# Kernel optimization log

Hardware: AMD Instinct MI355X
Metric: run time of the kernel (lower is better)

Reference implementation:

```python
import jax, jax.numpy as jnp
import numpy as np

B, L, D, H = 2, 2048, 768, 12
HD = D // H  # 64
BASE = 10000


def rope_tables(seq_len, head_dim, base):
    # inverse frequencies over even indices, angles [L, hd/2] -> duplicated to [L, hd]
    inv_freq = 1.0 / (base ** (jnp.arange(0, head_dim, 2, dtype=jnp.float32) / head_dim))
    angles = jnp.arange(seq_len, dtype=jnp.float32)[:, None] * inv_freq[None, :]
    cos = jnp.concatenate([jnp.cos(angles), jnp.cos(angles)], axis=-1)  # [L, hd]
    sin = jnp.concatenate([jnp.sin(angles), jnp.sin(angles)], axis=-1)
    return cos, sin


def rotate_half(x):
    x1, x2 = jnp.split(x, 2, axis=-1)
    return jnp.concatenate([-x2, x1], axis=-1)


def setup_inputs() -> dict:
    key = jax.random.key(0)
    k0, k1, k2 = jax.random.split(key, 3)
    s = 0.02
    return {
        "input_embeddings": jax.random.normal(k0, (B, L, D), dtype=jnp.float32),
        "w_qkv": jax.random.normal(k1, (D, 3 * D), dtype=jnp.float32) * s,
        "b_qkv": jnp.zeros((3 * D,), dtype=jnp.float32),
        "w_out": jax.random.normal(k2, (D, D), dtype=jnp.float32) * s,
        "b_out": jnp.zeros((D,), dtype=jnp.float32),
    }


def reference(input_embeddings, w_qkv, b_qkv, w_out, b_out):
    # QKV projection and head split: b l (h d) -> b h l d
    qkv = input_embeddings @ w_qkv + b_qkv
    q, k, v = jnp.split(qkv, 3, axis=-1)
    to_heads = lambda t: t.reshape(B, L, H, HD).transpose(0, 2, 1, 3)
    q, k, v = map(to_heads, (q, k, v))

    # RoPE (start_pos=0, no kv cache)
    cos, sin = rope_tables(L, HD, BASE)  # [L, HD], broadcasts over b,h
    q = q * cos + rotate_half(q) * sin
    k = k * cos + rotate_half(k) * sin

    # NOTE: source divides by sqrt(d.size(3)) = sqrt(key_seq_len), not sqrt(head_dim)
    scores = jnp.einsum("bhqd,bhkd->bhqk", q, k) / jnp.sqrt(jnp.float32(L))

    causal_mask = jnp.triu(jnp.ones((L, L), dtype=bool), 1)
    neg_inf = -jnp.finfo(scores.dtype).max
    scores = jnp.where(causal_mask, neg_inf, scores)

    probs = jax.nn.softmax(scores, axis=-1)  # dropout disabled (eval)
    attn_out = jnp.einsum("bhqk,bhkd->bhqd", probs, v)
    attn_out = attn_out.transpose(0, 2, 1, 3).reshape(B, L, D)  # b h l d -> b l (h d)
    output = attn_out @ w_out + b_out
    return output, probs
```

## Files before the change

kernel.cpp:

```cpp
#include <hip/hip_runtime.h>
#include <math.h>

#define B_  2
#define L_  2048
#define D_  768
#define H_  12
#define HD_ 64
#define M_  (B_*L_)
#define N3_ (3*D_)
#define OUT_ELEMS ((size_t)B_*L_*D_)

static constexpr float kScale = 0.022097086912079608f;
static constexpr float kLog2_10000_div32 = 0.415241011860920f;

typedef __attribute__((ext_vector_type(8))) short short8;
typedef __attribute__((ext_vector_type(4))) float f32x4;
typedef __attribute__((ext_vector_type(4))) unsigned short us4;

__device__ __forceinline__ unsigned short f2bf(float f) {
  union { float f; unsigned u; } v; v.f = f;
  unsigned r = v.u + 0x7FFFu + ((v.u >> 16) & 1u);
  return (unsigned short)(r >> 16);
}

__device__ __forceinline__ void async_cp16(const void* g, void* l) {
  __builtin_amdgcn_global_load_lds((const __attribute__((address_space(1))) void*)g,
                                   (__attribute__((address_space(3))) void*)l, 16, 0, 0);
}

__global__ __launch_bounds__(256) void bf16conv_kernel(const float* __restrict__ in,
                                                       unsigned short* __restrict__ out)
{
  const int idx = blockIdx.x * 256 + threadIdx.x;
  const float* src = in + (size_t)idx * 8;
  float4 a = *(const float4*)src;
  float4 b = *(const float4*)(src + 4);
  unsigned short t[8];
  t[0] = f2bf(a.x); t[1] = f2bf(a.y); t[2] = f2bf(a.z); t[3] = f2bf(a.w);
  t[4] = f2bf(b.x); t[5] = f2bf(b.y); t[6] = f2bf(b.z); t[7] = f2bf(b.w);
  *(uint4*)(out + (size_t)idx * 8) = *(uint4*)t;
}

__global__ __launch_bounds__(256) void wtrans_kernel(const float* __restrict__ in,
                                                     unsigned short* __restrict__ out,
                                                     int K, int N)
{
  __shared__ __align__(16) unsigned short T[64][72];
  const int n0 = blockIdx.x * 64;
  const int k0 = blockIdx.y * 64;
  const int tid = threadIdx.x;
  const int row = tid >> 2;
  const int col = (tid & 3) * 16;
  {
    const float* src = in + (size_t)(k0 + row) * N + n0 + col;
    unsigned short tmp[16];
#pragma unroll
    for (int j = 0; j < 16; j += 4) {
      float4 v = *(const float4*)(src + j);
      tmp[j] = f2bf(v.x); tmp[j + 1] = f2bf(v.y); tmp[j + 2] = f2bf(v.z); tmp[j + 3] = f2bf(v.w);
    }
    *(uint4*)&T[row][col]     = *(uint4*)tmp;
    *(uint4*)&T[row][col + 8] = *(uint4*)(tmp + 8);
  }
  __syncthreads();
  unsigned short tmp[16];
#pragma unroll
  for (int j = 0; j < 16; ++j) tmp[j] = T[col + j][row];
  unsigned short* dst = out + (size_t)(n0 + row) * K + k0 + col;
  *(uint4*)dst       = *(uint4*)tmp;
  *(uint4*)(dst + 8) = *(uint4*)(tmp + 8);
}

__global__ __launch_bounds__(256) void vtrans_kernel(const unsigned short* __restrict__ vb,
                                                     unsigned short* __restrict__ vt)
{
  __shared__ __align__(16) unsigned short T[64][72];
  const int bh = blockIdx.y;
  const int l0 = blockIdx.x * 64;
  const int tid = threadIdx.x;
  const int row = tid >> 2;
  const int col = (tid & 3) * 16;
  {
    const unsigned short* src = vb + ((size_t)bh * L_ + l0 + row) * HD_ + col;
    *(uint4*)&T[row][col]     = *(const uint4*)src;
    *(uint4*)&T[row][col + 8] = *(const uint4*)(src + 8);
  }
  __syncthreads();
  unsigned short tmp[16];
#pragma unroll
  for (int j = 0; j < 16; ++j) tmp[j] = T[col + j][row];
  unsigned short* dst = vt + ((size_t)bh * HD_ + row) * L_ + l0 + col;
  *(uint4*)dst       = *(uint4*)tmp;
  *(uint4*)(dst + 8) = *(uint4*)(tmp + 8);
}

__global__ __launch_bounds__(256) void gemm_mfma_kernel(
    const unsigned short* __restrict__ A, const unsigned short* __restrict__ Bt,
    const float* __restrict__ bias, float* __restrict__ C,
    int M, int N, int K, int mode,
    unsigned short* __restrict__ qp, unsigned short* __restrict__ kp,
    unsigned short* __restrict__ vp)
{
  __shared__ __align__(16) unsigned short As[2][128 * 32];
  __shared__ __align__(16) unsigned short Bs[2][128 * 32];

  const int tid  = threadIdx.x;
  const int w    = tid >> 6;
  const int lane = tid & 63;
  const int m16  = lane & 15;
  const int quad = lane >> 4;
  const int wr   = w & 1;
  const int wc   = w >> 1;

  const int bm = blockIdx.y * 128;
  const int bn = blockIdx.x * 128;

  const int s0 = w * 128 + lane;
  const int s1 = s0 + 64;
  const int r0 = s0 >> 2, c0 = (s0 & 3) ^ (r0 & 3);
  const int r1 = s1 >> 2, c1 = (s1 & 3) ^ (r1 & 3);
  const unsigned short* gA0 = A + (size_t)(bm + r0) * K + c0 * 8;
  const unsigned short* gA1 = A + (size_t)(bm + r1) * K + c1 * 8;
  const unsigned short* gB0 = Bt + (size_t)(bn + r0) * K + c0 * 8;
  const unsigned short* gB1 = Bt + (size_t)(bn + r1) * K + c1 * 8;
  const int oS0 = (w * 128) * 8;
  const int oS1 = (w * 128 + 64) * 8;

  const int sw = quad ^ (m16 & 3);
  int offA[4], offB[4];
#pragma unroll
  for (int i = 0; i < 4; ++i) {
    const int ra = wr * 64 + i * 16 + m16;
    const int rb = wc * 64 + i * 16 + m16;
    offA[i] = ra * 32 + sw * 8;
    offB[i] = rb * 32 + sw * 8;
  }

  f32x4 acc[4][4];
#pragma unroll
  for (int i = 0; i < 4; ++i)
#pragma unroll
    for (int j = 0; j < 4; ++j) { acc[i][j][0] = 0.f; acc[i][j][1] = 0.f; acc[i][j][2] = 0.f; acc[i][j][3] = 0.f; }

  async_cp16(gA0, &As[0][oS0]);
  async_cp16(gA1, &As[0][oS1]);
  async_cp16(gB0, &Bs[0][oS0]);
  async_cp16(gB1, &Bs[0][oS1]);
  __syncthreads();

  int cur = 0;
  for (int k0 = 0; k0 < K; k0 += 32) {
    const int nk = k0 + 32;
    if (nk < K) {
      unsigned short* an = &As[cur ^ 1][0];
      unsigned short* bn2 = &Bs[cur ^ 1][0];
      async_cp16(gA0 + nk, an + oS0);
      async_cp16(gA1 + nk, an + oS1);
      async_cp16(gB0 + nk, bn2 + oS0);
      async_cp16(gB1 + nk, bn2 + oS1);
    }
    const unsigned short* Ac = &As[cur][0];
    const unsigned short* Bc = &Bs[cur][0];
    short8 af[4], bfr[4];
#pragma unroll
    for (int i = 0; i < 4; ++i) {
      af[i]  = *(const short8*)(Ac + offA[i]);
      bfr[i] = *(const short8*)(Bc + offB[i]);
    }
#pragma unroll
    for (int i = 0; i < 4; ++i)
#pragma unroll
      for (int j = 0; j < 4; ++j)
        acc[i][j] = __builtin_amdgcn_mfma_f32_16x16x32_bf16(af[i], bfr[j], acc[i][j], 0, 0, 0);
    __syncthreads();
    cur ^= 1;
  }

  if (mode == 0) {
#pragma unroll
    for (int j = 0; j < 4; ++j) {
      const int n = bn + wc * 64 + j * 16 + m16;
      const float bj = bias[n];
#pragma unroll
      for (int i = 0; i < 4; ++i) {
        const int mrow = bm + wr * 64 + i * 16 + quad * 4;
#pragma unroll
        for (int r2 = 0; r2 < 4; ++r2)
          C[(size_t)(mrow + r2) * N + n] = acc[i][j][r2] + bj;
      }
    }
  } else {
    const int segbase = bn + wc * 64;
    const int which = segbase / D_;
    const int h = (segbase - which * D_) >> 6;
    unsigned short* dstT = (which == 0) ? qp : (which == 1) ? kp : vp;
    float bj[4];
#pragma unroll
    for (int og = 0; og < 4; ++og) bj[og] = bias[segbase + og * 16 + m16];
    const float invfA = exp2f(-(float)m16 * kLog2_10000_div32);
    const float invfB = exp2f(-(float)(16 + m16) * kLog2_10000_div32);

#pragma unroll
    for (int i = 0; i < 4; ++i) {
      const int mrow = bm + wr * 64 + i * 16 + quad * 4;
#pragma unroll
      for (int r2 = 0; r2 < 4; ++r2) {
        const int m = mrow + r2;
        const int bi = m >> 11;
        const int li = m & (L_ - 1);
        float vals[4];
#pragma unroll
        for (int og = 0; og < 4; ++og) vals[og] = acc[i][og][r2] + bj[og];
        unsigned short* drow = dstT + (((size_t)(bi * H_ + h)) * L_ + li) * HD_;
        if (which == 2) {
#pragma unroll
          for (int og = 0; og < 4; ++og) drow[og * 16 + m16] = f2bf(vals[og]);
        } else {
          const float fl = (float)li;
#pragma unroll
          for (int og = 0; og < 4; ++og) {
            const int d = og * 16 + m16;
            const float theta = fl * ((og & 1) ? invfB : invfA);
            float sv, cv;
            __sincosf(theta, &sv, &cv);
            const float part = vals[og ^ 2];
            const float rot = (og < 2) ? -part : part;
            drow[d] = f2bf(vals[og] * cv + rot * sv);
          }
        }
      }
    }
  }
}

__global__ __launch_bounds__(256) void attn_mfma_kernel(
    const unsigned short* __restrict__ qb, const unsigned short* __restrict__ kb,
    const unsigned short* __restrict__ vt, float* __restrict__ probs,
    unsigned short* __restrict__ attnb)
{
  __shared__ __align__(16) unsigned short Ks[2][64 * 64];
  __shared__ __align__(16) unsigned short Vs[2][64 * 64];
  __shared__ __align__(16) unsigned short Pb[4][16][72];

  const int tid  = threadIdx.x;
  const int w    = tid >> 6;
  const int lane = tid & 63;
  const int m16  = lane & 15;
  const int quad = lane >> 4;

  const int bh = blockIdx.y;
  const int qt = (int)gridDim.x - 1 - (int)blockIdx.x;
  const int q0 = qt * 64;
  const int bb = bh / H_;
  const int hh = bh - bb * H_;
  const int ktiles = qt + 1;
  const int qrow_base = q0 + w * 16;
  const int qrow = qrow_base + m16;

  const unsigned short* kbase = kb + (size_t)bh * L_ * HD_;
  const unsigned short* vbase = vt + (size_t)bh * HD_ * L_;

  const unsigned short* qp = qb + ((size_t)bh * L_ + qrow) * HD_ + quad * 8;
  const short8 qf0 = *(const short8*)(qp);
  const short8 qf1 = *(const short8*)(qp + 32);

  const int s0g = tid, s1g = tid + 256;
  const int r0 = s0g >> 3, c0 = (s0g & 7) ^ (r0 & 7);
  const int r1 = s1g >> 3, c1 = (s1g & 7) ^ (r1 & 7);
  const unsigned short* gK0 = kbase + (size_t)r0 * HD_ + c0 * 8;
  const unsigned short* gK1 = kbase + (size_t)r1 * HD_ + c1 * 8;
  const unsigned short* gV0 = vbase + (size_t)r0 * L_ + c0 * 8;
  const unsigned short* gV1 = vbase + (size_t)r1 * L_ + c1 * 8;
  const int oL0 = (w * 64) * 8;
  const int oL1 = (256 + w * 64) * 8;
  const int swk = m16 & 7;

  float lsum = 0.f;
  {
    async_cp16(gK0, &Ks[0][oL0]);
    async_cp16(gK1, &Ks[0][oL1]);
    __syncthreads();
    int cur = 0;
    for (int kt = 0; kt < ktiles; ++kt) {
      const int k0 = kt * 64;
      if (kt + 1 < ktiles) {
        const size_t adv = (size_t)(kt + 1) * 64 * HD_;
        async_cp16(gK0 + adv, &Ks[cur ^ 1][oL0]);
        async_cp16(gK1 + adv, &Ks[cur ^ 1][oL1]);
      }
      const unsigned short* Kc = &Ks[cur][0];
#pragma unroll
      for (int cg = 0; cg < 4; ++cg) {
        const int r = cg * 16 + m16;
        const short8 b0 = *(const short8*)(Kc + r * 64 + ((quad ^ swk) * 8));
        const short8 b1 = *(const short8*)(Kc + r * 64 + (((quad + 4) ^ swk) * 8));
        f32x4 s = {0.f, 0.f, 0.f, 0.f};
        s = __builtin_amdgcn_mfma_f32_16x16x32_bf16(b0, qf0, s, 0, 0, 0);
        s = __builtin_amdgcn_mfma_f32_16x16x32_bf16(b1, qf1, s, 0, 0, 0);
        const int kb2 = k0 + cg * 16 + quad * 4;
#pragma unroll
        for (int r2 = 0; r2 < 4; ++r2) {
          const float e = __expf(s[r2] * kScale);
          lsum += (kb2 + r2 <= qrow) ? e : 0.f;
        }
      }
      __syncthreads();
      cur ^= 1;
    }
  }
  lsum += __shfl_xor(lsum, 16, 64);
  lsum += __shfl_xor(lsum, 32, 64);
  const float linv = 1.f / lsum;

  f32x4 oacc[4];
#pragma unroll
  for (int og = 0; og < 4; ++og) { oacc[og][0]=0.f; oacc[og][1]=0.f; oacc[og][2]=0.f; oacc[og][3]=0.f; }

  float* const prow = probs + ((size_t)bh * L_ + qrow) * L_;

  {
    async_cp16(gK0, &Ks[0][oL0]);
    async_cp16(gK1, &Ks[0][oL1]);
    async_cp16(gV0, &Vs[0][oL0]);
    async_cp16(gV1, &Vs[0][oL1]);
    __syncthreads();
    int cur = 0;
    for (int kt = 0; kt < ktiles; ++kt) {
      const int k0 = kt * 64;
      if (kt + 1 < ktiles) {
        const size_t advK = (size_t)(kt + 1) * 64 * HD_;
        const int advV = (kt + 1) * 64;
        async_cp16(gK0 + advK, &Ks[cur ^ 1][oL0]);
        async_cp16(gK1 + advK, &Ks[cur ^ 1][oL1]);
        async_cp16(gV0 + advV, &Vs[cur ^ 1][oL0]);
        async_cp16(gV1 + advV, &Vs[cur ^ 1][oL1]);
      }
      const unsigned short* Kc = &Ks[cur][0];
      const unsigned short* Vc = &Vs[cur][0];
#pragma unroll
      for (int cg = 0; cg < 4; ++cg) {
        const int r = cg * 16 + m16;
        const short8 b0 = *(const short8*)(Kc + r * 64 + ((quad ^ swk) * 8));
        const short8 b1 = *(const short8*)(Kc + r * 64 + (((quad + 4) ^ swk) * 8));
        f32x4 s = {0.f, 0.f, 0.f, 0.f};
        s = __builtin_amdgcn_mfma_f32_16x16x32_bf16(b0, qf0, s, 0, 0, 0);
        s = __builtin_amdgcn_mfma_f32_16x16x32_bf16(b1, qf1, s, 0, 0, 0);
        const int cb = cg * 16 + quad * 4;
        const int kb2 = k0 + cb;
        f32x4 pv;
        us4 pb;
#pragma unroll
        for (int r2 = 0; r2 < 4; ++r2) {
          const float p = (kb2 + r2 <= qrow) ? __expf(s[r2] * kScale) * linv : 0.f;
          pv[r2] = p;
          pb[r2] = f2bf(p);
        }
        *(f32x4*)(prow + kb2) = pv;
        *(us4*)(&Pb[w][m16][cb]) = pb;
      }
      const short8 pa0 = *(const short8*)&Pb[w][m16][quad * 8];
      const short8 pa1 = *(const short8*)&Pb[w][m16][32 + quad * 8];
      __builtin_amdgcn_s_setprio(1);
#pragma unroll
      for (int og = 0; og < 4; ++og) {
        const int r = og * 16 + m16;
        const short8 v0 = *(const short8*)(Vc + r * 64 + ((quad ^ swk) * 8));
        const short8 v1 = *(const short8*)(Vc + r * 64 + (((quad + 4) ^ swk) * 8));
        oacc[og] = __builtin_amdgcn_mfma_f32_16x16x32_bf16(v0, pa0, oacc[og], 0, 0, 0);
        oacc[og] = __builtin_amdgcn_mfma_f32_16x16x32_bf16(v1, pa1, oacc[og], 0, 0, 0);
      }
      __builtin_amdgcn_s_setprio(0);
      __syncthreads();
      cur ^= 1;
    }
  }

#pragma unroll
  for (int og = 0; og < 4; ++og) {
    us4 o4;
#pragma unroll
    for (int r2 = 0; r2 < 4; ++r2) o4[r2] = f2bf(oacc[og][r2]);
    *(us4*)(attnb + ((size_t)bb * L_ + qrow) * D_ + hh * HD_ + og * 16 + quad * 4) = o4;
  }

  {
    const f32x4 z4 = {0.f, 0.f, 0.f, 0.f};
    for (int c0z = ktiles * 64; c0z < L_; c0z += 64) {
#pragma unroll
      for (int j = 0; j < 4; ++j)
        *(f32x4*)(prow + c0z + j * 16 + quad * 4) = z4;
    }
  }
}

extern "C" void kernel_launch(void* const* d_in, const int* in_sizes, int n_in,
                              void* d_out, int out_size, void* d_ws, size_t ws_size,
                              hipStream_t stream)
{
  const float* x     = (const float*)d_in[0];
  const float* w_qkv = (const float*)d_in[1];
  const float* b_qkv = (const float*)d_in[2];
  const float* w_out = (const float*)d_in[3];
  const float* b_out = (const float*)d_in[4];

  float* out   = (float*)d_out;
  float* probs = out + OUT_ELEMS;

  const size_t NE = (size_t)B_ * H_ * L_ * HD_;
  unsigned short* qbw   = (unsigned short*)d_ws;
  unsigned short* kbw   = qbw + NE;
  unsigned short* vbw   = kbw + NE;
  unsigned short* vtw   = vbw + NE;
  unsigned short* xbw   = vtw + NE;
  unsigned short* attnb = xbw + NE;
  unsigned short* wqT   = attnb + NE;
  unsigned short* woT   = wqT + (size_t)N3_ * D_;

  bf16conv_kernel<<<(int)(OUT_ELEMS / 8 / 256), 256, 0, stream>>>(x, xbw);
  wtrans_kernel<<<dim3(N3_ / 64, D_ / 64), 256, 0, stream>>>(w_qkv, wqT, D_, N3_);
  wtrans_kernel<<<dim3(D_ / 64, D_ / 64), 256, 0, stream>>>(w_out, woT, D_, D_);

  gemm_mfma_kernel<<<dim3(N3_ / 128, M_ / 128), 256, 0, stream>>>(
      xbw, wqT, b_qkv, nullptr, M_, N3_, D_, 1, qbw, kbw, vbw);

  vtrans_kernel<<<dim3(L_ / 64, B_ * H_), 256, 0, stream>>>(vbw, vtw);

  attn_mfma_kernel<<<dim3(L_ / 64, B_ * H_), 256, 0, stream>>>(qbw, kbw, vtw, probs, attnb);

  gemm_mfma_kernel<<<dim3(D_ / 128, M_ / 128), 256, 0, stream>>>(
      attnb, woT, b_out, out, M_, D_, D_, 0, nullptr, nullptr, nullptr);
}
```

Baseline: 550.5 us.

## Enlarge attention query tile to 128 rows with 512-thread blocks

The attention kernel now processes 128 query rows per block using 8 waves (512 threads) instead of 64 rows with 4 waves. Each K/V tile loaded into shared memory is reused by twice as many query rows, which halves K/V global traffic per query. Each thread now copies one 16-byte chunk per tile instead of two. The trade-off is fewer blocks, coarser causal load balance and more per-block resources. The diagonal tiles also carry more masked work, since each 128-row block scans up to its last 64-column tile.

```diff
diff --git a/kernel.cpp b/kernel.cpp
--- a/kernel.cpp
+++ b/kernel.cpp
@@ -233,14 +233,14 @@
   }
 }
 
-__global__ __launch_bounds__(256) void attn_mfma_kernel(
+__global__ __launch_bounds__(512) void attn_mfma_kernel(
     const unsigned short* __restrict__ qb, const unsigned short* __restrict__ kb,
     const unsigned short* __restrict__ vt, float* __restrict__ probs,
     unsigned short* __restrict__ attnb)
 {
   __shared__ __align__(16) unsigned short Ks[2][64 * 64];
   __shared__ __align__(16) unsigned short Vs[2][64 * 64];
-  __shared__ __align__(16) unsigned short Pb[4][16][72];
+  __shared__ __align__(16) unsigned short Pb[8][16][72];
 
   const int tid  = threadIdx.x;
   const int w    = tid >> 6;
@@ -250,12 +250,11 @@
 
   const int bh = blockIdx.y;
   const int qt = (int)gridDim.x - 1 - (int)blockIdx.x;
-  const int q0 = qt * 64;
+  const int q0 = qt * 128;
   const int bb = bh / H_;
   const int hh = bh - bb * H_;
-  const int ktiles = qt + 1;
-  const int qrow_base = q0 + w * 16;
-  const int qrow = qrow_base + m16;
+  const int ktiles = 2 * qt + 2;
+  const int qrow = q0 + w * 16 + m16;
 
   const unsigned short* kbase = kb + (size_t)bh * L_ * HD_;
   const unsigned short* vbase = vt + (size_t)bh * HD_ * L_;
@@ -264,29 +263,23 @@
   const short8 qf0 = *(const short8*)(qp);
   const short8 qf1 = *(const short8*)(qp + 32);
 
-  const int s0g = tid, s1g = tid + 256;
-  const int r0 = s0g >> 3, c0 = (s0g & 7) ^ (r0 & 7);
-  const int r1 = s1g >> 3, c1 = (s1g & 7) ^ (r1 & 7);
+  const int r0 = tid >> 3;
+  const int c0 = (tid & 7) ^ (r0 & 7);
   const unsigned short* gK0 = kbase + (size_t)r0 * HD_ + c0 * 8;
-  const unsigned short* gK1 = kbase + (size_t)r1 * HD_ + c1 * 8;
   const unsigned short* gV0 = vbase + (size_t)r0 * L_ + c0 * 8;
-  const unsigned short* gV1 = vbase + (size_t)r1 * L_ + c1 * 8;
-  const int oL0 = (w * 64) * 8;
-  const int oL1 = (256 + w * 64) * 8;
+  const int oL = (w * 64) * 8;
   const int swk = m16 & 7;
 
   float lsum = 0.f;
   {
-    async_cp16(gK0, &Ks[0][oL0]);
-    async_cp16(gK1, &Ks[0][oL1]);
+    async_cp16(gK0, &Ks[0][oL]);
     __syncthreads();
     int cur = 0;
     for (int kt = 0; kt < ktiles; ++kt) {
       const int k0 = kt * 64;
       if (kt + 1 < ktiles) {
         const size_t adv = (size_t)(kt + 1) * 64 * HD_;
-        async_cp16(gK0 + adv, &Ks[cur ^ 1][oL0]);
-        async_cp16(gK1 + adv, &Ks[cur ^ 1][oL1]);
+        async_cp16(gK0 + adv, &Ks[cur ^ 1][oL]);
       }
       const unsigned short* Kc = &Ks[cur][0];
 #pragma unroll
@@ -319,10 +312,8 @@
   float* const prow = probs + ((size_t)bh * L_ + qrow) * L_;
 
   {
-    async_cp16(gK0, &Ks[0][oL0]);
-    async_cp16(gK1, &Ks[0][oL1]);
-    async_cp16(gV0, &Vs[0][oL0]);
-    async_cp16(gV1, &Vs[0][oL1]);
+    async_cp16(gK0, &Ks[0][oL]);
+    async_cp16(gV0, &Vs[0][oL]);
     __syncthreads();
     int cur = 0;
     for (int kt = 0; kt < ktiles; ++kt) {
@@ -330,10 +321,8 @@
       if (kt + 1 < ktiles) {
         const size_t advK = (size_t)(kt + 1) * 64 * HD_;
         const int advV = (kt + 1) * 64;
-        async_cp16(gK0 + advK, &Ks[cur ^ 1][oL0]);
-        async_cp16(gK1 + advK, &Ks[cur ^ 1][oL1]);
-        async_cp16(gV0 + advV, &Vs[cur ^ 1][oL0]);
-        async_cp16(gV1 + advV, &Vs[cur ^ 1][oL1]);
+        async_cp16(gK0 + advK, &Ks[cur ^ 1][oL]);
+        async_cp16(gV0 + advV, &Vs[cur ^ 1][oL]);
       }
       const unsigned short* Kc = &Ks[cur][0];
       const unsigned short* Vc = &Vs[cur][0];
@@ -425,7 +414,7 @@
 
   vtrans_kernel<<<dim3(L_ / 64, B_ * H_), 256, 0, stream>>>(vbw, vtw);
 
-  attn_mfma_kernel<<<dim3(L_ / 64, B_ * H_), 256, 0, stream>>>(qbw, kbw, vtw, probs, attnb);
+  attn_mfma_kernel<<<dim3(L_ / 128, B_ * H_), 512, 0, stream>>>(qbw, kbw, vtw, probs, attnb);
 
   gemm_mfma_kernel<<<dim3(D_ / 128, M_ / 128), 256, 0, stream>>>(
       attnb, woT, b_out, out, M_, D_, D_, 0, nullptr, nullptr, nullptr);
```

Result: no change. 552.9 us (+0.4%).
